# Kernel optimization log

Hardware: AMD Instinct MI355X
Metric: run time of the kernel (lower is better)

Reference implementation:

```python
import jax, jax.numpy as jnp
import numpy as np

B, O, E, D, H = 8192, 64, 16, 16, 4  # batch, num_orbital, num_electron, n_bf_dets, hidden


def setup_inputs() -> dict:
    key = jax.random.key(0)
    ks = jax.random.split(key, 6)
    # occupation vectors: exactly E ones among O orbitals per sample
    scores = jax.random.uniform(ks[0], (B, O))
    occ_idx = jnp.argsort(scores, axis=1)[:, :E]  # (B, E) random occupied positions
    x = jnp.zeros((B, O), jnp.float32).at[jnp.arange(B)[:, None], occ_idx].set(1.0)
    # hidden MLP (positive_random_init kernels, zero bias as in flax default)
    W1 = jax.random.uniform(ks[1], (O, H), jnp.float32, minval=1.0, maxval=1.1)
    b1 = jnp.zeros((H,), jnp.float32)
    W2 = jax.random.uniform(ks[2], (H, H), jnp.float32, minval=1.0, maxval=1.1)
    b2 = jnp.zeros((H,), jnp.float32)
    # DenseGeneral: H -> (D, O, E)
    Wg = jax.random.normal(ks[3], (H, D, O, E), jnp.float32) / np.float32(np.sqrt(H))
    bg = jnp.zeros((D, O, E), jnp.float32)
    # bf_det_params: lecun_normal on (D, 1)
    bf_det_params = jax.random.normal(ks[4], (D, 1), jnp.float32) / np.float32(np.sqrt(D))
    return dict(x=x, W1=W1, b1=b1, W2=W2, b2=b2, Wg=Wg, bg=bg,
                bf_det_params=bf_det_params)


def reference(x, W1, b1, W2, b2, Wg, bg, bf_det_params):
    num_e = Wg.shape[-1]
    # indices of first num_e nonzero orbitals per sample (fill 0, like jnp.nonzero size=)
    sel = jax.vmap(lambda r: jnp.nonzero(r, size=num_e, fill_value=0)[0])(x)  # (B, E)
    # tiny MLP with relu
    h = jax.nn.relu(x @ W1 + b1)          # (B, H)
    h = jax.nn.relu(h @ W2 + b2)          # (B, H)
    # DenseGeneral projection to (B, D, O, E)
    y = jnp.einsum('bh,hdoe->bdoe', h, Wg) + bg
    # gather occupied-orbital rows -> (B, D, E, E)
    g = jax.vmap(lambda yi, si: yi[:, si, :])(y, sel)
    dets = jnp.linalg.det(g)              # (B, D)
    out = (dets @ bf_det_params)[:, 0]    # (B,)
    # zero out samples whose selected indices sum to 0 (empty/degenerate config)
    return jnp.where(jnp.sum(sel, axis=1) == 0, jnp.float32(0.0), out)
```

## Files before the change

kernel.cpp:

```cpp
#include <hip/hip_runtime.h>


template <int CTRL>
__device__ __forceinline__ float dpp_movf(float v) {
    return __int_as_float(__builtin_amdgcn_update_dpp(
        0, __float_as_int(v), CTRL, 0xF, 0xF, true));
}

__global__ __launch_bounds__(128) void backflow_kernel(
    const float* __restrict__ x,
    const float* __restrict__ W1,
    const float* __restrict__ b1,
    const float* __restrict__ W2,
    const float* __restrict__ b2,
    const float* __restrict__ Wg,
    const float* __restrict__ bg,
    const float* __restrict__ bf,
    float* __restrict__ out,
    int B)
{
    const int lane  = threadIdx.x & 63;
    const int wavei = threadIdx.x >> 6;
    const int b     = blockIdx.x * 2 + wavei;
    const int d = lane >> 2;
    const int l = lane & 3;

    __shared__ float4 smem[1024];
    __shared__ int s_retry;
    float4* const sm = smem + (wavei << 9);
    if (threadIdx.x == 0) s_retry = 0;
    if (b >= B) return;

    const float xv = x[b * 64 + lane];
    const unsigned long long mask = __ballot(xv != 0.0f);
    const bool empty = ((mask & ~1ull) == 0ull);

    const float4 w1 = reinterpret_cast<const float4*>(W1)[lane];
    float c0 = xv * w1.x, c1 = xv * w1.y, c2 = xv * w1.z, c3 = xv * w1.w;
    #pragma unroll
    for (int off = 32; off >= 1; off >>= 1) {
        c0 += __shfl_xor(c0, off);
        c1 += __shfl_xor(c1, off);
        c2 += __shfl_xor(c2, off);
        c3 += __shfl_xor(c3, off);
    }
    const float h10 = fmaxf(c0 + b1[0], 0.0f);
    const float h11 = fmaxf(c1 + b1[1], 0.0f);
    const float h12 = fmaxf(c2 + b1[2], 0.0f);
    const float h13 = fmaxf(c3 + b1[3], 0.0f);

    float h2[4];
    #pragma unroll
    for (int j = 0; j < 4; ++j) {
        float v = b2[j];
        v = fmaf(h10, W2[0 * 4 + j], v);
        v = fmaf(h11, W2[1 * 4 + j], v);
        v = fmaf(h12, W2[2 * 4 + j], v);
        v = fmaf(h13, W2[3 * 4 + j], v);
        h2[j] = fmaxf(v, 0.0f);
    }

    unsigned long long mr = mask;
    #pragma unroll
    for (int i = 0; i < 15; ++i) if (i < d) mr &= mr - 1;
    const int selr = mr ? (int)__builtin_ctzll(mr) : 0;
    const int rowoff = selr * 4 + l;

    const float4* wgp = reinterpret_cast<const float4*>(Wg);
    const float4* bgp = reinterpret_cast<const float4*>(bg);

    float R0[16], R1[16], R2[16], R3[16];

#define STAGE_ONE(DS) do {                                                   \
        const int _ds = (DS);                                                \
        const float4 wb  = bgp[_ds * 256 + rowoff];                          \
        const float4 w3  = wgp[(48 + _ds) * 256 + rowoff];                   \
        const float4 w2c = wgp[(32 + _ds) * 256 + rowoff];                   \
        const float4 wv1 = wgp[(16 + _ds) * 256 + rowoff];                   \
        const float4 w0  = wgp[_ds * 256 + rowoff];                          \
        float4 a;                                                            \
        a.x = fmaf(h2[0],w0.x, fmaf(h2[1],wv1.x, fmaf(h2[2],w2c.x, fmaf(h2[3],w3.x, wb.x)))); \
        a.y = fmaf(h2[0],w0.y, fmaf(h2[1],wv1.y, fmaf(h2[2],w2c.y, fmaf(h2[3],w3.y, wb.y)))); \
        a.z = fmaf(h2[0],w0.z, fmaf(h2[1],wv1.z, fmaf(h2[2],w2c.z, fmaf(h2[3],w3.z, wb.z)))); \
        a.w = fmaf(h2[0],w0.w, fmaf(h2[1],wv1.w, fmaf(h2[2],w2c.w, fmaf(h2[3],w3.w, wb.w)))); \
        sm[(_ds & 7) * 64 + d * 4 + (l ^ (_ds & 3))] = a;                    \
    } while (0)

#define RD_ROWS(RW, S) do { _Pragma("unroll")                                \
        for (int q = 0; q < 4; ++q) {                                        \
            const float4 t = sm[(d & 7) * 64 + (l + 4 * (S)) * 4 + (q ^ (d & 3))]; \
            RW[q*4+0] = t.x; RW[q*4+1] = t.y;                                \
            RW[q*4+2] = t.z; RW[q*4+3] = t.w;                                \
        } } while (0)

#define STAGE_AND_READ do {                                                  \
        _Pragma("unroll 1")                                                  \
        for (int half = 0; half < 2; ++half) {                               \
            _Pragma("unroll 1")                                              \
            for (int dp = 0; dp < 4; ++dp) {           \
                STAGE_ONE(half * 8 + 2 * dp);                                \
                STAGE_ONE(half * 8 + 2 * dp + 1);                            \
                __builtin_amdgcn_sched_barrier(0);                           \
            }                                                                \
            __syncthreads();                                                 \
            if ((d >> 3) == half) {                                          \
                RD_ROWS(R0, 0);                                              \
                RD_ROWS(R1, 1);                                              \
                RD_ROWS(R2, 2);                                              \
                RD_ROWS(R3, 3);                                              \
            }                                                                \
            __syncthreads();                                                 \
        } } while (0)

#define STEP4(K, DAC, PA, PB, PC, PD) do {                                   \
        const float pivot = dpp_movf<((K) & 3) * 0x55>(PA[0]);               \
        nb += !(fabsf(pivot) >= tau);                                        \
        DAC *= (double)pivot;                                                \
        const float pinv = __builtin_amdgcn_rcpf(pivot);                     \
        const float fa = (l > ((K) & 3)) ? PA[0] * pinv : 0.0f;              \
        const float fb = PB[0] * pinv;                                       \
        const float fc = PC[0] * pinv;                                       \
        const float fd = PD[0] * pinv;                                       \
        _Pragma("unroll")                                                    \
        for (int j = 1; j <= 15 - (K); ++j) {                                \
            const float pv = dpp_movf<((K) & 3) * 0x55>(PA[j]);              \
            PA[j - 1] = fmaf(-fa, pv, PA[j]);                                \
            PB[j - 1] = fmaf(-fb, pv, PB[j]);                                \
            PC[j - 1] = fmaf(-fc, pv, PC[j]);                                \
            PD[j - 1] = fmaf(-fd, pv, PD[j]);                                \
        } } while (0)

#define STEP3(K, DAC, PA, PB, PC) do {                                       \
        const float pivot = dpp_movf<((K) & 3) * 0x55>(PA[0]);               \
        nb += !(fabsf(pivot) >= tau);                                        \
        DAC *= (double)pivot;                                                \
        const float pinv = __builtin_amdgcn_rcpf(pivot);                     \
        const float fa = (l > ((K) & 3)) ? PA[0] * pinv : 0.0f;              \
        const float fb = PB[0] * pinv;                                       \
        const float fc = PC[0] * pinv;                                       \
        _Pragma("unroll")                                                    \
        for (int j = 1; j <= 15 - (K); ++j) {                                \
            const float pv = dpp_movf<((K) & 3) * 0x55>(PA[j]);              \
            PA[j - 1] = fmaf(-fa, pv, PA[j]);                                \
            PB[j - 1] = fmaf(-fb, pv, PB[j]);                                \
            PC[j - 1] = fmaf(-fc, pv, PC[j]);                                \
        } } while (0)

#define STEP2(K, DAC, PA, PB) do {                                           \
        const float pivot = dpp_movf<((K) & 3) * 0x55>(PA[0]);               \
        nb += !(fabsf(pivot) >= tau);                                        \
        DAC *= (double)pivot;                                                \
        const float pinv = __builtin_amdgcn_rcpf(pivot);                     \
        const float fa = (l > ((K) & 3)) ? PA[0] * pinv : 0.0f;              \
        const float fb = PB[0] * pinv;                                       \
        _Pragma("unroll")                                                    \
        for (int j = 1; j <= 15 - (K); ++j) {                                \
            const float pv = dpp_movf<((K) & 3) * 0x55>(PA[j]);              \
            PA[j - 1] = fmaf(-fa, pv, PA[j]);                                \
            PB[j - 1] = fmaf(-fb, pv, PB[j]);                                \
        } } while (0)

#define STEP1(K, DAC, PA) do {                                               \
        const float pivot = dpp_movf<((K) & 3) * 0x55>(PA[0]);               \
        nb += !(fabsf(pivot) >= tau);                                        \
        DAC *= (double)pivot;                                                \
        const float pinv = __builtin_amdgcn_rcpf(pivot);                     \
        const float fa = (l > ((K) & 3)) ? PA[0] * pinv : 0.0f;              \
        _Pragma("unroll")                                                    \
        for (int j = 1; j <= 15 - (K); ++j) {                                \
            const float pv = dpp_movf<((K) & 3) * 0x55>(PA[j]);              \
            PA[j - 1] = fmaf(-fa, pv, PA[j]);                                \
        } } while (0)

    double deta = 1.0, detb = 1.0;
    bool domix = false;

    #pragma unroll 1
    for (int attempt = 0; attempt < 2; ++attempt) {
        STAGE_AND_READ;

        if (domix) {
            const bool z = (l == 0);
            #pragma unroll
            for (int j = 0; j < 16; ++j) {
                const float w0 = z ? R1[j] : R0[j];
                const float wv = z ? R2[j] : R1[j];
                const float w2 = z ? R3[j] : R2[j];
                const float w3 = z ? R0[j] : R3[j];
                R0[j] = fmaf(0.5f, dpp_movf<0x39>(w0), R0[j]);
                R1[j] = fmaf(0.5f, dpp_movf<0x39>(wv), R1[j]);
                R2[j] = fmaf(0.5f, dpp_movf<0x39>(w2), R2[j]);
                R3[j] = fmaf(0.5f, dpp_movf<0x39>(w3), R3[j]);
            }
        }

        float mm = 0.0f;
        #pragma unroll
        for (int j = 0; j < 16; ++j) {
            mm = fmaxf(mm, fmaxf(fmaxf(fabsf(R0[j]), fabsf(R1[j])),
                                 fmaxf(fabsf(R2[j]), fabsf(R3[j]))));
        }
        mm = fmaxf(mm, dpp_movf<0xB1>(mm));
        mm = fmaxf(mm, dpp_movf<0x4E>(mm));
        const float tau = 1e-4f * mm;

        deta = 1.0; detb = 1.0;
        int nb = 0;

        STEP4(0,  deta, R0, R1, R2, R3);
        STEP4(1,  detb, R0, R1, R2, R3);
        STEP4(2,  deta, R0, R1, R2, R3);
        STEP4(3,  detb, R0, R1, R2, R3);
        STEP3(4,  deta, R1, R2, R3);
        STEP3(5,  detb, R1, R2, R3);
        STEP3(6,  deta, R1, R2, R3);
        STEP3(7,  detb, R1, R2, R3);
        STEP2(8,  deta, R2, R3);
        STEP2(9,  detb, R2, R3);
        STEP2(10, deta, R2, R3);
        STEP2(11, detb, R2, R3);
        STEP1(12, deta, R3);
        STEP1(13, detb, R3);
        STEP1(14, deta, R3);
        STEP1(15, detb, R3);

        if (attempt == 0) {
            if (nb != 0) s_retry = 1;
            __syncthreads();
            if (!s_retry) break;
            domix = (nb != 0);
        }
    }
#undef STEP1
#undef STEP2
#undef STEP3
#undef STEP4
#undef STAGE_AND_READ
#undef RD_ROWS
#undef STAGE_ONE

    float detf = (float)(deta * detb);
    if (domix) detf *= (65536.0f / 65535.0f);
    float acc = (l == 0) ? detf * bf[d] : 0.0f;
    acc += __shfl_xor(acc, 4);
    acc += __shfl_xor(acc, 8);
    acc += __shfl_xor(acc, 16);
    acc += __shfl_xor(acc, 32);
    if (lane == 0) out[b] = empty ? 0.0f : acc;
}

extern "C" void kernel_launch(void* const* d_in, const int* in_sizes, int n_in,
                              void* d_out, int out_size, void* d_ws, size_t ws_size,
                              hipStream_t stream) {
    const float* x  = (const float*)d_in[0];
    const float* W1 = (const float*)d_in[1];
    const float* b1 = (const float*)d_in[2];
    const float* W2 = (const float*)d_in[3];
    const float* b2 = (const float*)d_in[4];
    const float* Wg = (const float*)d_in[5];
    const float* bg = (const float*)d_in[6];
    const float* bf = (const float*)d_in[7];
    float* out = (float*)d_out;

    const int B = in_sizes[0] / 64;
    const int blocks = (B + 1) / 2;
    backflow_kernel<<<blocks, 128, 0, stream>>>(x, W1, b1, W2, b2, Wg, bg, bf, out, B);
}
```

Baseline: 47.00 us.

## Use 1024-thread blocks with per-slice double-buffered LDS staging and wave-local retry

Moves from 2 waves per block to 16 waves per block. Each wave now stages one D-slice at a time into a small two-slot LDS ring and reads it right away, instead of staging eight slices and then reading. This cuts LDS per wave from 8 KB to 2 KB. The block-wide retry flag becomes a wave-local __any vote. The cost is a __syncthreads per slice across 16 waves in the first attempt, and the second attempt runs without barriers, which relies on wave-local ordering.

New measurement: 74.14 us. 1.58x slower.

```diff
diff --git a/kernel.cpp b/kernel.cpp
--- a/kernel.cpp
+++ b/kernel.cpp
@@ -7,7 +7,7 @@
         0, __float_as_int(v), CTRL, 0xF, 0xF, true));
 }
 
-__global__ __launch_bounds__(128) void backflow_kernel(
+__global__ __launch_bounds__(1024) void backflow_kernel(
     const float* __restrict__ x,
     const float* __restrict__ W1,
     const float* __restrict__ b1,
@@ -21,15 +21,14 @@
 {
     const int lane  = threadIdx.x & 63;
     const int wavei = threadIdx.x >> 6;
-    const int b     = blockIdx.x * 2 + wavei;
+    const int borig = blockIdx.x * 16 + wavei;
+    const bool bok  = (borig < B);
+    const int b     = bok ? borig : (B - 1);
     const int d = lane >> 2;
     const int l = lane & 3;
 
-    __shared__ float4 smem[1024];
-    __shared__ int s_retry;
-    float4* const sm = smem + (wavei << 9);
-    if (threadIdx.x == 0) s_retry = 0;
-    if (b >= B) return;
+    __shared__ float4 smem[16 * 128];
+    float4* const sm = smem + (wavei << 7);
 
     const float xv = x[b * 64 + lane];
     const unsigned long long mask = __ballot(xv != 0.0f);
@@ -83,33 +82,14 @@
         a.y = fmaf(h2[0],w0.y, fmaf(h2[1],wv1.y, fmaf(h2[2],w2c.y, fmaf(h2[3],w3.y, wb.y)))); \
         a.z = fmaf(h2[0],w0.z, fmaf(h2[1],wv1.z, fmaf(h2[2],w2c.z, fmaf(h2[3],w3.z, wb.z)))); \
         a.w = fmaf(h2[0],w0.w, fmaf(h2[1],wv1.w, fmaf(h2[2],w2c.w, fmaf(h2[3],w3.w, wb.w)))); \
-        sm[(_ds & 7) * 64 + d * 4 + (l ^ (_ds & 3))] = a;                    \
+        sm[((_ds & 1) << 6) + d * 4 + (l ^ (_ds & 3))] = a;                  \
     } while (0)
 
-#define RD_ROWS(RW, S) do { _Pragma("unroll")                                \
+#define RD_ROWS(RW, S, DS) do { _Pragma("unroll")                            \
         for (int q = 0; q < 4; ++q) {                                        \
-            const float4 t = sm[(d & 7) * 64 + (l + 4 * (S)) * 4 + (q ^ (d & 3))]; \
+            const float4 t = sm[(((DS) & 1) << 6) + (l + 4 * (S)) * 4 + (q ^ ((DS) & 3))]; \
             RW[q*4+0] = t.x; RW[q*4+1] = t.y;                                \
             RW[q*4+2] = t.z; RW[q*4+3] = t.w;                                \
-        } } while (0)
-
-#define STAGE_AND_READ do {                                                  \
-        _Pragma("unroll 1")                                                  \
-        for (int half = 0; half < 2; ++half) {                               \
-            _Pragma("unroll 1")                                              \
-            for (int dp = 0; dp < 4; ++dp) {           \
-                STAGE_ONE(half * 8 + 2 * dp);                                \
-                STAGE_ONE(half * 8 + 2 * dp + 1);                            \
-                __builtin_amdgcn_sched_barrier(0);                           \
-            }                                                                \
-            __syncthreads();                                                 \
-            if ((d >> 3) == half) {                                          \
-                RD_ROWS(R0, 0);                                              \
-                RD_ROWS(R1, 1);                                              \
-                RD_ROWS(R2, 2);                                              \
-                RD_ROWS(R3, 3);                                              \
-            }                                                                \
-            __syncthreads();                                                 \
         } } while (0)
 
 #define STEP4(K, DAC, PA, PB, PC, PD) do {                                   \
@@ -177,7 +157,18 @@
 
     #pragma unroll 1
     for (int attempt = 0; attempt < 2; ++attempt) {
-        STAGE_AND_READ;
+        #pragma unroll 1
+        for (int ds = 0; ds < 16; ++ds) {
+            STAGE_ONE(ds);
+            __builtin_amdgcn_sched_barrier(0);
+            if (attempt == 0) __syncthreads();
+            if (d == ds) {
+                RD_ROWS(R0, 0, ds);
+                RD_ROWS(R1, 1, ds);
+                RD_ROWS(R2, 2, ds);
+                RD_ROWS(R3, 3, ds);
+            }
+        }
 
         if (domix) {
             const bool z = (l == 0);
@@ -225,9 +216,7 @@
         STEP1(15, detb, R3);
 
         if (attempt == 0) {
-            if (nb != 0) s_retry = 1;
-            __syncthreads();
-            if (!s_retry) break;
+            if (!__any(nb != 0)) break;
             domix = (nb != 0);
         }
     }
@@ -235,7 +224,6 @@
 #undef STEP2
 #undef STEP3
 #undef STEP4
-#undef STAGE_AND_READ
 #undef RD_ROWS
 #undef STAGE_ONE
 
@@ -246,7 +234,7 @@
     acc += __shfl_xor(acc, 8);
     acc += __shfl_xor(acc, 16);
     acc += __shfl_xor(acc, 32);
-    if (lane == 0) out[b] = empty ? 0.0f : acc;
+    if (lane == 0 && bok) out[b] = empty ? 0.0f : acc;
 }
 
 extern "C" void kernel_launch(void* const* d_in, const int* in_sizes, int n_in,
@@ -263,6 +251,6 @@
     float* out = (float*)d_out;
 
     const int B = in_sizes[0] / 64;
-    const int blocks = (B + 1) / 2;
-    backflow_kernel<<<blocks, 128, 0, stream>>>(x, W1, b1, W2, b2, Wg, bg, bf, out, B);
+    const int blocks = (B + 15) / 16;
+    backflow_kernel<<<blocks, 1024, 0, stream>>>(x, W1, b1, W2, b2, Wg, bg, bf, out, B);
 }
```
